# Performance work log

Hardware: AMD Instinct MI355X
Metric: run time of the kernel (lower is better)

## Reference

```python
import jax, jax.numpy as jnp
import numpy as np

B, D, H = 131072, 8, 128


def setup_inputs() -> dict:
    key = jax.random.key(0)
    ks = jax.random.split(key, 8)
    s1 = 1.0 / np.sqrt(D + 1)
    s2 = 1.0 / np.sqrt(H)
    return {
        "z": jax.random.normal(ks[0], (B, D), dtype=jnp.float32),
        "logp_z": jnp.zeros((B, 1), dtype=jnp.float32),
        "t": jax.random.uniform(ks[1], (1,), dtype=jnp.float32),
        "W1": jax.random.normal(ks[2], (D + 1, H), dtype=jnp.float32) * s1,
        "b1": jnp.zeros((H,), dtype=jnp.float32),
        "W2": jax.random.normal(ks[3], (H, H), dtype=jnp.float32) * s2,
        "b2": jnp.zeros((H,), dtype=jnp.float32),
        "W3": jax.random.normal(ks[4], (H, D), dtype=jnp.float32) * s2,
        "b3": jnp.zeros((D,), dtype=jnp.float32),
    }


def _net_single(z_i, t_scalar, W1, b1, W2, b2, W3, b3):
    # z_i: [D] -> dz/dt: [D]; FFJORD-style MLP on concat([z, t])
    x = jnp.concatenate([z_i, t_scalar[None]])  # [D+1]
    h = jnp.tanh(x @ W1 + b1)
    h = jnp.tanh(h @ W2 + b2)
    return h @ W3 + b3


def reference(z, logp_z, t, W1, b1, W2, b2, W3, b3):
    t_scalar = t.reshape(())

    def f_i(z_i):
        return _net_single(z_i, t_scalar, W1, b1, W2, b2, W3, b3)

    # dz/dt for every sample (batched forward)
    dz_dt = jax.vmap(f_i)(z)  # [B, D]
    # Exact Jacobian trace: fused forward-mode batched Jacobian (replaces the
    # original's D sequential autograd.grad reverse-mode calls)
    jac = jax.vmap(jax.jacfwd(f_i))(z)  # [B, D, D]
    trace = jnp.einsum("bii->b", jac)  # [B]
    dlogp_z_dt = -trace[:, None]  # [B, 1]
    return (dz_dt, dlogp_z_dt)
```

## Files before the change

### kernel.cpp

```cpp
#include <hip/hip_runtime.h>
#include <hip/hip_bf16.h>

#define BATCH 131072
#define PITCH_H 72

typedef __bf16 bf16x8 __attribute__((ext_vector_type(8)));
typedef float floatx4 __attribute__((ext_vector_type(4)));

__device__ __forceinline__ float fast_tanh(float x) {
    float e = __expf(2.0f * x);
    return 1.0f - 2.0f * __builtin_amdgcn_rcpf(e + 1.0f);
}


__global__ void prep_kernel(const float* __restrict__ W1,
                            const float* __restrict__ W2,
                            const float* __restrict__ W3,
                            __bf16* __restrict__ ws) {
    int idx = blockIdx.x * 256 + threadIdx.x;
    if (idx < 16384) {
        int j = idx & 7, q = (idx >> 3) & 3, n = (idx >> 5) & 127, kb = idx >> 12;
        int k = kb * 32 + q * 8 + j;
        ws[idx] = (__bf16)W2[k * 128 + n];
        float c = 0.0f;
        #pragma unroll
        for (int d = 0; d < 8; ++d) c += W3[k * 8 + d] * W1[d * 128 + n];
        ws[16384 + idx] = (__bf16)(W2[n * 128 + k] * c);
    } else if (idx < 20480) {
        int t = idx - 16384;
        int j = t & 7, q = (t >> 3) & 3, n = t >> 5;
        int k = q * 8 + j;
        ws[32768 + t] = (k < 9) ? (__bf16)W1[k * 128 + n] : (__bf16)0.0f;
    } else if (idx < 22528) {
        int t = idx - 20480;
        int j = t & 7, q = (t >> 3) & 3, n = (t >> 5) & 15, kb = t >> 9;
        int k = kb * 32 + q * 8 + j;
        ws[36864 + t] = (n < 8) ? (__bf16)W3[k * 8 + n] : (__bf16)0.0f;
    }
}


__device__ __forceinline__ void phase0_h1(
        const bf16x8& ax, const bf16x8* w1f, const float* sb1,
        __bf16* T, int p, int q, float* a1c, bf16x8* ah) {
    #pragma unroll
    for (int half = 0; half < 2; ++half) {
        #pragma unroll
        for (int lt = 0; lt < 4; ++lt) {
            const int nt = half * 4 + lt;
            const int n = nt * 16 + p;
            floatx4 acc = {0.f, 0.f, 0.f, 0.f};
            acc = __builtin_amdgcn_mfma_f32_16x16x32_bf16(ax, w1f[nt], acc, 0, 0, 0);
            const float bn = sb1[n];
            #pragma unroll
            for (int r = 0; r < 4; ++r) {
                const float h1 = fast_tanh(acc[r] + bn);
                a1c[nt * 4 + r] = __builtin_fmaf(-h1, h1, 1.0f);
                T[(q * 4 + r) * PITCH_H + lt * 16 + p] = (__bf16)h1;
            }
        }
        ah[half * 2 + 0] = *(const bf16x8*)&T[p * PITCH_H + q * 8];
        ah[half * 2 + 1] = *(const bf16x8*)&T[p * PITCH_H + 32 + q * 8];
    }
}

__device__ __forceinline__ void phase1_h2(
        const bf16x8* ah, const bf16x8* W2sv, const float* sb2,
        __bf16* T, int p, int q, bf16x8* ah2, bf16x8* aa) {
    #pragma unroll
    for (int half = 0; half < 2; ++half) {
        #pragma unroll
        for (int lt = 0; lt < 4; ++lt) {
            const int nt = half * 4 + lt;
            const int n = nt * 16 + p;
            floatx4 acc = {0.f, 0.f, 0.f, 0.f};
            #pragma unroll
            for (int kb = 0; kb < 4; ++kb)
                acc = __builtin_amdgcn_mfma_f32_16x16x32_bf16(
                        ah[kb], W2sv[(kb * 128 + n) * 4 + q], acc, 0, 0, 0);
            const float bn = sb2[n];
            #pragma unroll
            for (int r = 0; r < 4; ++r) {
                const float h2 = fast_tanh(acc[r] + bn);
                T[(q * 4 + r) * PITCH_H + lt * 16 + p] = (__bf16)h2;
            }
        }
        ah2[half * 2 + 0] = *(const bf16x8*)&T[p * PITCH_H + q * 8];
        ah2[half * 2 + 1] = *(const bf16x8*)&T[p * PITCH_H + 32 + q * 8];
    }
    #pragma unroll
    for (int kb = 0; kb < 4; ++kb) {
        #pragma unroll
        for (int j = 0; j < 8; ++j) {
            const float f = (float)ah2[kb][j];
            aa[kb][j] = (__bf16)__builtin_fmaf(-f, f, 1.0f);
        }
    }
}

__device__ __forceinline__ void phase3_dz(
        const bf16x8* ah2, const bf16x8* w3f, float b3v,
        int s0, int p, int q, float* out) {
    floatx4 acc3 = {0.f, 0.f, 0.f, 0.f};
    #pragma unroll
    for (int kb = 0; kb < 4; ++kb)
        acc3 = __builtin_amdgcn_mfma_f32_16x16x32_bf16(ah2[kb], w3f[kb], acc3, 0, 0, 0);
    if (p < 8) {
        #pragma unroll
        for (int r = 0; r < 4; ++r)
            out[(size_t)(s0 + q * 4 + r) * 8 + p] = acc3[r] + b3v;
    }
}

__device__ __forceinline__ void phase2_tr(
        const bf16x8* aa, const float* a1c, const bf16x8* GTsv,
        int s0, int p, int q, float* out) {
    float tr[4] = {0.f, 0.f, 0.f, 0.f};
    #pragma unroll
    for (int nt = 0; nt < 8; ++nt) {
        const int n = nt * 16 + p;
        floatx4 acc = {0.f, 0.f, 0.f, 0.f};
        #pragma unroll
        for (int kb = 0; kb < 4; ++kb)
            acc = __builtin_amdgcn_mfma_f32_16x16x32_bf16(
                    aa[kb], GTsv[(kb * 128 + n) * 4 + q], acc, 0, 0, 0);
        #pragma unroll
        for (int r = 0; r < 4; ++r)
            tr[r] = __builtin_fmaf(a1c[nt * 4 + r], acc[r], tr[r]);
    }
    #pragma unroll
    for (int r = 0; r < 4; ++r) {
        float v = tr[r];
        v += __shfl_xor(v, 1, 64);
        v += __shfl_xor(v, 2, 64);
        v += __shfl_xor(v, 4, 64);
        v += __shfl_xor(v, 8, 64);
        tr[r] = v;
    }
    if (p == 0) {
        #pragma unroll
        for (int r = 0; r < 4; ++r)
            out[(size_t)BATCH * 8 + s0 + q * 4 + r] = -tr[r];
    }
}

__global__ __launch_bounds__(256, 2) void cnf_main(
        const float* __restrict__ z, const float* __restrict__ t_ptr,
        const float* __restrict__ b1g, const float* __restrict__ b2g,
        const float* __restrict__ b3g, const __bf16* __restrict__ ws,
        float* __restrict__ out) {
    __shared__ __bf16 sW2s[16384];
    __shared__ __bf16 sGTs[16384];
    __shared__ float sb1[128];
    __shared__ float sb2[128];
    __shared__ __bf16 tile[4][16 * PITCH_H];

    const int tid = threadIdx.x;
    const int lane = tid & 63;
    const int w = tid >> 6;
    const int p = lane & 15;
    const int q = lane >> 4;
    const int sbase = blockIdx.x * 128 + w * 32;
    const float tval = t_ptr[0];

    bf16x8 ax0, ax1;
    #pragma unroll
    for (int j = 0; j < 8; ++j) { ax0[j] = (__bf16)0.0f; ax1[j] = (__bf16)0.0f; }
    if (q == 0) {
        const float4* zp0 = (const float4*)(z + (size_t)(sbase + p) * 8);
        const float4* zp1 = (const float4*)(z + (size_t)(sbase + 16 + p) * 8);
        const float4 a0 = zp0[0], a1 = zp0[1], c0 = zp1[0], c1 = zp1[1];
        ax0[0] = (__bf16)a0.x; ax0[1] = (__bf16)a0.y;
        ax0[2] = (__bf16)a0.z; ax0[3] = (__bf16)a0.w;
        ax0[4] = (__bf16)a1.x; ax0[5] = (__bf16)a1.y;
        ax0[6] = (__bf16)a1.z; ax0[7] = (__bf16)a1.w;
        ax1[0] = (__bf16)c0.x; ax1[1] = (__bf16)c0.y;
        ax1[2] = (__bf16)c0.z; ax1[3] = (__bf16)c0.w;
        ax1[4] = (__bf16)c1.x; ax1[5] = (__bf16)c1.y;
        ax1[6] = (__bf16)c1.z; ax1[7] = (__bf16)c1.w;
    } else if (q == 1) {
        ax0[0] = (__bf16)tval;
        ax1[0] = (__bf16)tval;
    }

    const bf16x8* W1g = (const bf16x8*)(ws + 32768);
    const bf16x8* W3g = (const bf16x8*)(ws + 36864);
    bf16x8 w1f[8];
    #pragma unroll
    for (int nt = 0; nt < 8; ++nt) w1f[nt] = W1g[(nt * 16 + p) * 4 + q];
    bf16x8 w3f[4];
    #pragma unroll
    for (int kb = 0; kb < 4; ++kb) w3f[kb] = W3g[(kb * 16 + p) * 4 + q];

    {
        uint4* dst = (uint4*)sW2s;
        const uint4* src = (const uint4*)ws;
        #pragma unroll
        for (int i = 0; i < 8; ++i) dst[tid + i * 256] = src[tid + i * 256];
        uint4* dstg = (uint4*)sGTs;
        const uint4* srcg = (const uint4*)(ws + 16384);
        #pragma unroll
        for (int i = 0; i < 8; ++i) dstg[tid + i * 256] = srcg[tid + i * 256];
        if (tid < 128) { sb1[tid] = b1g[tid]; sb2[tid] = b2g[tid]; }
    }
    __syncthreads();

    __bf16* T = tile[w];
    const bf16x8* W2sv = (const bf16x8*)sW2s;
    const bf16x8* GTsv = (const bf16x8*)sGTs;
    const float b3v = (p < 8) ? b3g[p] : 0.0f;
    const int s0a = sbase;
    const int s0b = sbase + 16;

    float a1c0[32], a1c1[32];
    bf16x8 ah0[4], ah1[4];
    phase0_h1(ax0, w1f, sb1, T, p, q, a1c0, ah0);
    phase0_h1(ax1, w1f, sb1, T, p, q, a1c1, ah1);

    bf16x8 ah2_0[4], aa0[4];
    phase1_h2(ah0, W2sv, sb2, T, p, q, ah2_0, aa0);
    phase3_dz(ah2_0, w3f, b3v, s0a, p, q, out);

    bf16x8 ah2_1[4], aa1[4];
    phase1_h2(ah1, W2sv, sb2, T, p, q, ah2_1, aa1);
    phase2_tr(aa0, a1c0, GTsv, s0a, p, q, out);

    phase3_dz(ah2_1, w3f, b3v, s0b, p, q, out);
    phase2_tr(aa1, a1c1, GTsv, s0b, p, q, out);
}

extern "C" void kernel_launch(void* const* d_in, const int* in_sizes, int n_in,
                              void* d_out, int out_size, void* d_ws, size_t ws_size,
                              hipStream_t stream) {
    const float* z  = (const float*)d_in[0];
    const float* t  = (const float*)d_in[2];
    const float* W1 = (const float*)d_in[3];
    const float* b1 = (const float*)d_in[4];
    const float* W2 = (const float*)d_in[5];
    const float* b2 = (const float*)d_in[6];
    const float* W3 = (const float*)d_in[7];
    const float* b3 = (const float*)d_in[8];
    __bf16* ws = (__bf16*)d_ws;
    float* out = (float*)d_out;

    prep_kernel<<<88, 256, 0, stream>>>(W1, W2, W3, ws);
    cnf_main<<<1024, 256, 0, stream>>>(z, t, b1, b2, b3, ws, out);
}
```

Before: 97.32 us.

## Interleave two sample tiles per wave and overlap layer-1 with weight staging

Restructures the main kernel so both 16-sample tiles of each wave are processed together in every phase, sharing each LDS weight fragment load across two MFMAs. Layer-1 computation now runs before the __syncthreads that waits for the W2/G copy into shared memory, so it can overlap the global-to-LDS staging. Biases move from shared memory to per-lane registers, and the transpose tiles shrink to 32-column chunks with separate buffers per tile. This raises register pressure, since two sets of activations and accumulators are live at once, and may reduce occupancy or cause spills.

```diff
diff --git a/kernel.cpp b/kernel.cpp
--- a/kernel.cpp
+++ b/kernel.cpp
@@ -2,7 +2,7 @@
 #include <hip/hip_bf16.h>
 
 #define BATCH 131072
-#define PITCH_H 72
+#define PITCH_Q 40
 
 typedef __bf16 bf16x8 __attribute__((ext_vector_type(8)));
 typedef float floatx4 __attribute__((ext_vector_type(4)));
@@ -39,111 +39,6 @@
     }
 }
 
-
-__device__ __forceinline__ void phase0_h1(
-        const bf16x8& ax, const bf16x8* w1f, const float* sb1,
-        __bf16* T, int p, int q, float* a1c, bf16x8* ah) {
-    #pragma unroll
-    for (int half = 0; half < 2; ++half) {
-        #pragma unroll
-        for (int lt = 0; lt < 4; ++lt) {
-            const int nt = half * 4 + lt;
-            const int n = nt * 16 + p;
-            floatx4 acc = {0.f, 0.f, 0.f, 0.f};
-            acc = __builtin_amdgcn_mfma_f32_16x16x32_bf16(ax, w1f[nt], acc, 0, 0, 0);
-            const float bn = sb1[n];
-            #pragma unroll
-            for (int r = 0; r < 4; ++r) {
-                const float h1 = fast_tanh(acc[r] + bn);
-                a1c[nt * 4 + r] = __builtin_fmaf(-h1, h1, 1.0f);
-                T[(q * 4 + r) * PITCH_H + lt * 16 + p] = (__bf16)h1;
-            }
-        }
-        ah[half * 2 + 0] = *(const bf16x8*)&T[p * PITCH_H + q * 8];
-        ah[half * 2 + 1] = *(const bf16x8*)&T[p * PITCH_H + 32 + q * 8];
-    }
-}
-
-__device__ __forceinline__ void phase1_h2(
-        const bf16x8* ah, const bf16x8* W2sv, const float* sb2,
-        __bf16* T, int p, int q, bf16x8* ah2, bf16x8* aa) {
-    #pragma unroll
-    for (int half = 0; half < 2; ++half) {
-        #pragma unroll
-        for (int lt = 0; lt < 4; ++lt) {
-            const int nt = half * 4 + lt;
-            const int n = nt * 16 + p;
-            floatx4 acc = {0.f, 0.f, 0.f, 0.f};
-            #pragma unroll
-            for (int kb = 0; kb < 4; ++kb)
-                acc = __builtin_amdgcn_mfma_f32_16x16x32_bf16(
-                        ah[kb], W2sv[(kb * 128 + n) * 4 + q], acc, 0, 0, 0);
-            const float bn = sb2[n];
-            #pragma unroll
-            for (int r = 0; r < 4; ++r) {
-                const float h2 = fast_tanh(acc[r] + bn);
-                T[(q * 4 + r) * PITCH_H + lt * 16 + p] = (__bf16)h2;
-            }
-        }
-        ah2[half * 2 + 0] = *(const bf16x8*)&T[p * PITCH_H + q * 8];
-        ah2[half * 2 + 1] = *(const bf16x8*)&T[p * PITCH_H + 32 + q * 8];
-    }
-    #pragma unroll
-    for (int kb = 0; kb < 4; ++kb) {
-        #pragma unroll
-        for (int j = 0; j < 8; ++j) {
-            const float f = (float)ah2[kb][j];
-            aa[kb][j] = (__bf16)__builtin_fmaf(-f, f, 1.0f);
-        }
-    }
-}
-
-__device__ __forceinline__ void phase3_dz(
-        const bf16x8* ah2, const bf16x8* w3f, float b3v,
-        int s0, int p, int q, float* out) {
-    floatx4 acc3 = {0.f, 0.f, 0.f, 0.f};
-    #pragma unroll
-    for (int kb = 0; kb < 4; ++kb)
-        acc3 = __builtin_amdgcn_mfma_f32_16x16x32_bf16(ah2[kb], w3f[kb], acc3, 0, 0, 0);
-    if (p < 8) {
-        #pragma unroll
-        for (int r = 0; r < 4; ++r)
-            out[(size_t)(s0 + q * 4 + r) * 8 + p] = acc3[r] + b3v;
-    }
-}
-
-__device__ __forceinline__ void phase2_tr(
-        const bf16x8* aa, const float* a1c, const bf16x8* GTsv,
-        int s0, int p, int q, float* out) {
-    float tr[4] = {0.f, 0.f, 0.f, 0.f};
-    #pragma unroll
-    for (int nt = 0; nt < 8; ++nt) {
-        const int n = nt * 16 + p;
-        floatx4 acc = {0.f, 0.f, 0.f, 0.f};
-        #pragma unroll
-        for (int kb = 0; kb < 4; ++kb)
-            acc = __builtin_amdgcn_mfma_f32_16x16x32_bf16(
-                    aa[kb], GTsv[(kb * 128 + n) * 4 + q], acc, 0, 0, 0);
-        #pragma unroll
-        for (int r = 0; r < 4; ++r)
-            tr[r] = __builtin_fmaf(a1c[nt * 4 + r], acc[r], tr[r]);
-    }
-    #pragma unroll
-    for (int r = 0; r < 4; ++r) {
-        float v = tr[r];
-        v += __shfl_xor(v, 1, 64);
-        v += __shfl_xor(v, 2, 64);
-        v += __shfl_xor(v, 4, 64);
-        v += __shfl_xor(v, 8, 64);
-        tr[r] = v;
-    }
-    if (p == 0) {
-        #pragma unroll
-        for (int r = 0; r < 4; ++r)
-            out[(size_t)BATCH * 8 + s0 + q * 4 + r] = -tr[r];
-    }
-}
-
 __global__ __launch_bounds__(256, 2) void cnf_main(
         const float* __restrict__ z, const float* __restrict__ t_ptr,
         const float* __restrict__ b1g, const float* __restrict__ b2g,
@@ -151,9 +46,7 @@
         float* __restrict__ out) {
     __shared__ __bf16 sW2s[16384];
     __shared__ __bf16 sGTs[16384];
-    __shared__ float sb1[128];
-    __shared__ float sb2[128];
-    __shared__ __bf16 tile[4][16 * PITCH_H];
+    __shared__ __align__(16) __bf16 tile[4][2][16 * PITCH_Q];
 
     const int tid = threadIdx.x;
     const int lane = tid & 63;
@@ -191,6 +84,10 @@
     bf16x8 w3f[4];
     #pragma unroll
     for (int kb = 0; kb < 4; ++kb) w3f[kb] = W3g[(kb * 16 + p) * 4 + q];
+    float b1f[8], b2f[8];
+    #pragma unroll
+    for (int nt = 0; nt < 8; ++nt) { b1f[nt] = b1g[nt * 16 + p]; b2f[nt] = b2g[nt * 16 + p]; }
+    const float b3v = (p < 8) ? b3g[p] : 0.0f;
 
     {
         uint4* dst = (uint4*)sW2s;
@@ -201,32 +98,141 @@
         const uint4* srcg = (const uint4*)(ws + 16384);
         #pragma unroll
         for (int i = 0; i < 8; ++i) dstg[tid + i * 256] = srcg[tid + i * 256];
-        if (tid < 128) { sb1[tid] = b1g[tid]; sb2[tid] = b2g[tid]; }
-    }
+    }
+
+    __bf16* Ta = tile[w][0];
+    __bf16* Tb = tile[w][1];
+
+    float a1c0[32], a1c1[32];
+    bf16x8 ah0[4], ah1[4];
+    #pragma unroll
+    for (int c = 0; c < 4; ++c) {
+        floatx4 aA[2], aB[2];
+        #pragma unroll
+        for (int lt = 0; lt < 2; ++lt) {
+            floatx4 zz = {0.f, 0.f, 0.f, 0.f};
+            aA[lt] = __builtin_amdgcn_mfma_f32_16x16x32_bf16(ax0, w1f[2 * c + lt], zz, 0, 0, 0);
+            aB[lt] = __builtin_amdgcn_mfma_f32_16x16x32_bf16(ax1, w1f[2 * c + lt], zz, 0, 0, 0);
+        }
+        #pragma unroll
+        for (int lt = 0; lt < 2; ++lt) {
+            const int nt = 2 * c + lt;
+            const float bn = b1f[nt];
+            #pragma unroll
+            for (int r = 0; r < 4; ++r) {
+                const float h1a = fast_tanh(aA[lt][r] + bn);
+                a1c0[nt * 4 + r] = __builtin_fmaf(-h1a, h1a, 1.0f);
+                Ta[(q * 4 + r) * PITCH_Q + lt * 16 + p] = (__bf16)h1a;
+                const float h1b = fast_tanh(aB[lt][r] + bn);
+                a1c1[nt * 4 + r] = __builtin_fmaf(-h1b, h1b, 1.0f);
+                Tb[(q * 4 + r) * PITCH_Q + lt * 16 + p] = (__bf16)h1b;
+            }
+        }
+        ah0[c] = *(const bf16x8*)&Ta[p * PITCH_Q + q * 8];
+        ah1[c] = *(const bf16x8*)&Tb[p * PITCH_Q + q * 8];
+    }
+
     __syncthreads();
-
-    __bf16* T = tile[w];
     const bf16x8* W2sv = (const bf16x8*)sW2s;
     const bf16x8* GTsv = (const bf16x8*)sGTs;
-    const float b3v = (p < 8) ? b3g[p] : 0.0f;
-    const int s0a = sbase;
-    const int s0b = sbase + 16;
-
-    float a1c0[32], a1c1[32];
-    bf16x8 ah0[4], ah1[4];
-    phase0_h1(ax0, w1f, sb1, T, p, q, a1c0, ah0);
-    phase0_h1(ax1, w1f, sb1, T, p, q, a1c1, ah1);
-
-    bf16x8 ah2_0[4], aa0[4];
-    phase1_h2(ah0, W2sv, sb2, T, p, q, ah2_0, aa0);
-    phase3_dz(ah2_0, w3f, b3v, s0a, p, q, out);
-
-    bf16x8 ah2_1[4], aa1[4];
-    phase1_h2(ah1, W2sv, sb2, T, p, q, ah2_1, aa1);
-    phase2_tr(aa0, a1c0, GTsv, s0a, p, q, out);
-
-    phase3_dz(ah2_1, w3f, b3v, s0b, p, q, out);
-    phase2_tr(aa1, a1c1, GTsv, s0b, p, q, out);
+
+    bf16x8 ah2_0[4], ah2_1[4];
+    #pragma unroll
+    for (int c = 0; c < 4; ++c) {
+        floatx4 aA[2] = {{0.f, 0.f, 0.f, 0.f}, {0.f, 0.f, 0.f, 0.f}};
+        floatx4 aB[2] = {{0.f, 0.f, 0.f, 0.f}, {0.f, 0.f, 0.f, 0.f}};
+        #pragma unroll
+        for (int kb = 0; kb < 4; ++kb) {
+            #pragma unroll
+            for (int lt = 0; lt < 2; ++lt) {
+                const int n = (2 * c + lt) * 16 + p;
+                const bf16x8 wf = W2sv[(kb * 128 + n) * 4 + q];
+                aA[lt] = __builtin_amdgcn_mfma_f32_16x16x32_bf16(ah0[kb], wf, aA[lt], 0, 0, 0);
+                aB[lt] = __builtin_amdgcn_mfma_f32_16x16x32_bf16(ah1[kb], wf, aB[lt], 0, 0, 0);
+            }
+        }
+        #pragma unroll
+        for (int lt = 0; lt < 2; ++lt) {
+            const int nt = 2 * c + lt;
+            const float bn = b2f[nt];
+            #pragma unroll
+            for (int r = 0; r < 4; ++r) {
+                const float h2a = fast_tanh(aA[lt][r] + bn);
+                Ta[(q * 4 + r) * PITCH_Q + lt * 16 + p] = (__bf16)h2a;
+                const float h2b = fast_tanh(aB[lt][r] + bn);
+                Tb[(q * 4 + r) * PITCH_Q + lt * 16 + p] = (__bf16)h2b;
+            }
+        }
+        ah2_0[c] = *(const bf16x8*)&Ta[p * PITCH_Q + q * 8];
+        ah2_1[c] = *(const bf16x8*)&Tb[p * PITCH_Q + q * 8];
+    }
+
+    floatx4 d3A = {0.f, 0.f, 0.f, 0.f}, d3B = {0.f, 0.f, 0.f, 0.f};
+    #pragma unroll
+    for (int kb = 0; kb < 4; ++kb) {
+        d3A = __builtin_amdgcn_mfma_f32_16x16x32_bf16(ah2_0[kb], w3f[kb], d3A, 0, 0, 0);
+        d3B = __builtin_amdgcn_mfma_f32_16x16x32_bf16(ah2_1[kb], w3f[kb], d3B, 0, 0, 0);
+    }
+    if (p < 8) {
+        #pragma unroll
+        for (int r = 0; r < 4; ++r) {
+            out[(size_t)(sbase + q * 4 + r) * 8 + p] = d3A[r] + b3v;
+            out[(size_t)(sbase + 16 + q * 4 + r) * 8 + p] = d3B[r] + b3v;
+        }
+    }
+
+    bf16x8 aa0[4], aa1[4];
+    #pragma unroll
+    for (int kb = 0; kb < 4; ++kb) {
+        #pragma unroll
+        for (int j = 0; j < 8; ++j) {
+            const float fa = (float)ah2_0[kb][j];
+            aa0[kb][j] = (__bf16)__builtin_fmaf(-fa, fa, 1.0f);
+            const float fb = (float)ah2_1[kb][j];
+            aa1[kb][j] = (__bf16)__builtin_fmaf(-fb, fb, 1.0f);
+        }
+    }
+
+    float trA[4] = {0.f, 0.f, 0.f, 0.f}, trB[4] = {0.f, 0.f, 0.f, 0.f};
+    #pragma unroll
+    for (int nt = 0; nt < 8; ++nt) {
+        const int n = nt * 16 + p;
+        floatx4 uA = {0.f, 0.f, 0.f, 0.f}, uB = {0.f, 0.f, 0.f, 0.f};
+        #pragma unroll
+        for (int kb = 0; kb < 4; ++kb) {
+            const bf16x8 gf = GTsv[(kb * 128 + n) * 4 + q];
+            uA = __builtin_amdgcn_mfma_f32_16x16x32_bf16(aa0[kb], gf, uA, 0, 0, 0);
+            uB = __builtin_amdgcn_mfma_f32_16x16x32_bf16(aa1[kb], gf, uB, 0, 0, 0);
+        }
+        #pragma unroll
+        for (int r = 0; r < 4; ++r) {
+            trA[r] = __builtin_fmaf(a1c0[nt * 4 + r], uA[r], trA[r]);
+            trB[r] = __builtin_fmaf(a1c1[nt * 4 + r], uB[r], trB[r]);
+        }
+    }
+
+    #pragma unroll
+    for (int r = 0; r < 4; ++r) {
+        float va = trA[r];
+        va += __shfl_xor(va, 1, 64);
+        va += __shfl_xor(va, 2, 64);
+        va += __shfl_xor(va, 4, 64);
+        va += __shfl_xor(va, 8, 64);
+        trA[r] = va;
+        float vb = trB[r];
+        vb += __shfl_xor(vb, 1, 64);
+        vb += __shfl_xor(vb, 2, 64);
+        vb += __shfl_xor(vb, 4, 64);
+        vb += __shfl_xor(vb, 8, 64);
+        trB[r] = vb;
+    }
+    if (p == 0) {
+        #pragma unroll
+        for (int r = 0; r < 4; ++r) {
+            out[(size_t)BATCH * 8 + sbase + q * 4 + r] = -trA[r];
+            out[(size_t)BATCH * 8 + sbase + 16 + q * 4 + r] = -trB[r];
+        }
+    }
 }
 
 extern "C" void kernel_launch(void* const* d_in, const int* in_sizes, int n_in,
```

Result: faster. 94.35 us (-3.0%).
